# Optimization experiments

Measured on AMD Instinct MI355X. Metric: run time of the kernel, lower is better.

Reference implementation:

```python
import jax, jax.numpy as jnp
import numpy as np

B, T_ENC, T_DEC = 1024, 96, 16
P_Q, CFG, H = 235, 32, 256
D_IN = P_Q + 5 + 10 + 3 + 3  # 256, matches input_size in __init__


def _lstm_step(x, h, c, Wih, Whh, bih, bhh):
    # torch.nn.LSTMCell: gate order i, f, g, o
    g = x @ Wih.T + bih + h @ Whh.T + bhh
    i, f, gg, o = jnp.split(g, 4, axis=-1)
    c2 = jax.nn.sigmoid(f) * c + jax.nn.sigmoid(i) * jnp.tanh(gg)
    h2 = jax.nn.sigmoid(o) * jnp.tanh(c2)
    return h2, c2


def setup_inputs():
    key = jax.random.key(0)
    ks = jax.random.split(key, 30)
    s = 0.05

    def n(i, shape):
        return jax.random.normal(ks[i], shape, jnp.float32) * s

    return {
        "input_p_q": jax.random.normal(ks[0], (B, T_ENC, P_Q), jnp.float32),
        "input_config": jax.random.normal(ks[1], (B, T_ENC, CFG), jnp.float32),
        "input_time": jax.random.randint(ks[2], (B, T_ENC, 3), 0, 5, jnp.int32),
        "W_cfg": n(3, (10, CFG)), "b_cfg": n(4, (10,)),
        "E_hour": n(5, (24, 5)), "E_wd": n(6, (8, 3)), "E_season": n(7, (5, 3)),
        "Wih_e": n(8, (4 * H, D_IN)), "Whh_e": n(9, (4 * H, H)),
        "bih_e": n(10, (4 * H,)), "bhh_e": n(11, (4 * H,)),
        "Wih_d": n(12, (4, H + 1)), "Whh_d": n(13, (4, 1)),
        "bih_d": n(14, (4,)), "bhh_d": n(15, (4,)),
        "Wi_s": n(16, (H, D_IN)), "bi_s": n(17, (H,)),
        "We_s": n(18, (H, 2 * H)),
        "Vd_s": n(19, (1, H)), "bVd_s": n(20, (1,)),
        "Wd_t": n(21, (H, H)), "bd_t": n(22, (H,)),
        "Wd2_t": n(23, (H, 2)),
        "Vd_t": n(24, (1, H)), "bVd_t": n(25, (1,)),
    }


def _forward(input_p_q, input_config, input_time, W_cfg, b_cfg, E_hour, E_wd, E_season,
             Wih_e, Whh_e, bih_e, bhh_e, Wih_d, Whh_d, bih_d, bhh_d,
             Wi_s, bi_s, We_s, Vd_s, bVd_s, Wd_t, bd_t, Wd2_t, Vd_t, bVd_t):
    b = input_p_q.shape[0]
    cfg = input_config @ W_cfg.T + b_cfg  # [B,T,10]
    inputs = jnp.concatenate([
        input_p_q, cfg,
        E_hour[input_time[:, :, 0]],
        E_wd[input_time[:, :, 1]],
        E_season[input_time[:, :, 2]],
    ], axis=2)  # [B,T,D_IN]

    # spatial_attention_Wi(inputs) hoisted out of the per-step loop (identical math)
    wi = inputs @ Wi_s.T + bi_s  # [B,T,H]

    def enc_step(carry, xt):
        hi, ci = carry
        x_t, wi_t = xt
        # Vd(tanh(We([h,c]) + Wi(x)))  -> [B,1] scalar gate (no softmax in original)
        a = jnp.tanh(jnp.concatenate([hi, ci], axis=1) @ We_s.T + wi_t) @ Vd_s.T + bVd_s
        h2, c2 = _lstm_step(x_t * a, hi, ci, Wih_e, Whh_e, bih_e, bhh_e)
        return (h2, c2), h2

    h0 = jnp.zeros((b, H), inputs.dtype)
    (_, _), mid = jax.lax.scan(enc_step, (h0, h0),
                               (inputs.transpose(1, 0, 2), wi.transpose(1, 0, 2)))
    mid = mid.transpose(1, 0, 2)  # [B,T,H]

    # temporal_attention_Wd(mid) does not depend on decode step -> hoisted
    wd_mid = mid @ Wd_t.T + bd_t  # [B,T,H]
    prev0 = mid[:, -1, 2:3]       # [B,1], as in original (element 2 of last hidden)

    def dec_step(carry, _):
        hi, ci, prev = carry
        q = jnp.concatenate([hi, ci], axis=1) @ Wd2_t.T       # [B,H]
        a = jnp.tanh(q[:, None, :] + wd_mid) @ Vd_t.T + bVd_t  # [B,T,1], raw scores
        ctx = jnp.einsum('bth,bt->bh', mid, a[..., 0])          # weighted sum over T
        h2, c2 = _lstm_step(jnp.concatenate([ctx, prev], axis=1), hi, ci,
                            Wih_d, Whh_d, bih_d, bhh_d)
        return (h2, c2, h2), h2

    z = jnp.zeros((b, 1), inputs.dtype)
    _, dec = jax.lax.scan(dec_step, (z, z, prev0), None, length=T_DEC)
    return dec.transpose(1, 0, 2)  # [B,16,1]


def reference(input_p_q, input_config, input_time, W_cfg, b_cfg, E_hour, E_wd, E_season,
              Wih_e, Whh_e, bih_e, bhh_e, Wih_d, Whh_d, bih_d, bhh_d,
              Wi_s, bi_s, We_s, Vd_s, bVd_s, Wd_t, bd_t, Wd2_t, Vd_t, bVd_t):
    return _forward(input_p_q, input_config, input_time, W_cfg, b_cfg, E_hour, E_wd,
                    E_season, Wih_e, Whh_e, bih_e, bhh_e, Wih_d, Whh_d, bih_d, bhh_d,
                    Wi_s, bi_s, We_s, Vd_s, bVd_s, Wd_t, bd_t, Wd2_t, Vd_t, bVd_t)
```

## Files before the change

kernel.cpp:

```cpp
#include <hip/hip_runtime.h>
#include <hip/hip_bf16.h>


typedef unsigned short ushort_t;
using short4v = __attribute__((ext_vector_type(4))) short;
using short8  = __attribute__((ext_vector_type(8))) short;
using floatx4 = __attribute__((ext_vector_type(4))) float;

#define DEVFN static __device__ __forceinline__

DEVFN float bs2f(ushort_t u) {
    union { float f; unsigned v; } c; c.v = ((unsigned)u) << 16; return c.f;
}
DEVFN ushort_t f2bs(float f) {
    __hip_bfloat16 h = __float2bfloat16(f);
    return *reinterpret_cast<ushort_t*>(&h);
}
DEVFN float gload(const void* p, long i, int bf) {
    if (bf) return bs2f(((const ushort_t*)p)[i]);
    return ((const float*)p)[i];
}
DEVFN float sigm(float x) { return 1.f / (1.f + __expf(-x)); }
DEVFN float ftanh(float x) {
    float t = __expf(-2.f * fabsf(x));
    float r = (1.f - t) / (1.f + t);
    return copysignf(r, x);
}
DEVFN short8 ld8(const ushort_t* p) { return *reinterpret_cast<const short8*>(p); }

DEVFN void bar_lgkm() {
    asm volatile("s_waitcnt lgkmcnt(0)" ::: "memory");
    __builtin_amdgcn_s_barrier();
}

DEVFN void gload_lds16(const ushort_t* g, ushort_t* l) {
    typedef const __attribute__((address_space(1))) unsigned int gu32;
    typedef __attribute__((address_space(3))) unsigned int lu32;
    __builtin_amdgcn_global_load_lds((gu32*)g, (lu32*)l, 16, 0, 0);
}

DEVFN const ushort_t* chunk_ptr(const ushort_t* wesW, const ushort_t* whhW, int j) {
    return (j < 16) ? (wesW + (j << 9)) : (whhW + ((j - 16) << 9));
}

struct SrcPtrs { const void* p[26]; };
struct WsPtrs {
    ushort_t *wcfg, *bcfg, *eh, *ew, *es, *wis, *bis, *wes, *vds, *bvds,
             *whh, *wih, *bih, *bhh, *wdt, *bdt, *wd2t, *vdt, *bvdt,
             *wihd, *whhd, *bihd, *bhhd;
};

__global__ void k_detect(const void* probe, int* flag) {
    if (threadIdx.x == 0 && blockIdx.x == 0) {
        const ushort_t* u = (const ushort_t*)probe;
        int ok = 1;
        for (int i = 0; i < 16; ++i) {
            ushort_t v = u[2 * i];
            int e = (v >> 7) & 0xFF;
            if (!(v == 0 || (e >= 96 && e <= 126))) ok = 0;
        }
        *flag = ok;
    }
}

__global__ __launch_bounds__(256) void k_cvt(SrcPtrs sp, WsPtrs wp, const int* flagp) {
    int bf = *flagp;
    const void* src = nullptr; ushort_t* dst = nullptr; long n = 0;
    switch (blockIdx.x) {
        case 0:  src = sp.p[3];  dst = wp.wcfg; n = 320;    break;
        case 1:  src = sp.p[4];  dst = wp.bcfg; n = 10;     break;
        case 2:  src = sp.p[5];  dst = wp.eh;   n = 120;    break;
        case 3:  src = sp.p[6];  dst = wp.ew;   n = 24;     break;
        case 4:  src = sp.p[7];  dst = wp.es;   n = 15;     break;
        case 5:  src = sp.p[16]; dst = wp.wis;  n = 65536;  break;
        case 6:  src = sp.p[17]; dst = wp.bis;  n = 256;    break;
        case 8:  src = sp.p[19]; dst = wp.vds;  n = 256;    break;
        case 9:  src = sp.p[20]; dst = wp.bvds; n = 1;      break;
        case 12: src = sp.p[10]; dst = wp.bih;  n = 1024;   break;
        case 13: src = sp.p[11]; dst = wp.bhh;  n = 1024;   break;
        case 14: src = sp.p[21]; dst = wp.wdt;  n = 65536;  break;
        case 15: src = sp.p[22]; dst = wp.bdt;  n = 256;    break;
        case 16: src = sp.p[23]; dst = wp.wd2t; n = 512;    break;
        case 17: src = sp.p[24]; dst = wp.vdt;  n = 256;    break;
        case 18: src = sp.p[25]; dst = wp.bvdt; n = 1;      break;
        case 19: src = sp.p[12]; dst = wp.wihd; n = 1028;   break;
        case 20: src = sp.p[13]; dst = wp.whhd; n = 4;      break;
        case 21: src = sp.p[14]; dst = wp.bihd; n = 4;      break;
        case 22: src = sp.p[15]; dst = wp.bhhd; n = 4;      break;
        default: return;
    }
    for (long i = threadIdx.x; i < n; i += 256) {
        float v = bf ? bs2f(((const ushort_t*)src)[i]) : ((const float*)src)[i];
        dst[i] = f2bs(v);
    }
}

__global__ __launch_bounds__(256) void k_permA(
    const void* whh_src, const void* wih_src,
    ushort_t* whhp, ushort_t* wihb, const int* flagp)
{
    int bf = *flagp;
    long base = (long)blockIdx.x * 2048;
    if (blockIdx.y == 1) {
#pragma unroll
        for (int ii = 0; ii < 8; ++ii) {
            long p = base + threadIdx.x + ii * 256;
            wihb[p] = f2bs(gload(wih_src, p, bf));
        }
        return;
    }
#pragma unroll
    for (int ii = 0; ii < 8; ++ii) {
        long p = base + threadIdx.x + ii * 256;
        int c = (int)(p >> 9), l = (int)((p >> 3) & 63), e = (int)(p & 7);
        int w = c >> 5, kk = (c >> 2) & 7, g = c & 3;
        int q = l >> 4, ln = l & 15;
        long si = (long)(g * 256 + w * 16 + ln) * 256 + kk * 32 + q * 8 + e;
        whhp[p] = f2bs(gload(whh_src, si, bf));
    }
}

__global__ __launch_bounds__(256) void k_permB(
    const void* wes_src, ushort_t* wesp, const int* flagp)
{
    int bf = *flagp;
    long base = (long)blockIdx.x * 2048;
#pragma unroll
    for (int ii = 0; ii < 8; ++ii) {
        long p = base + threadIdx.x + ii * 256;
        int c = (int)(p >> 9), l = (int)((p >> 3) & 63), e = (int)(p & 7);
        int w = c >> 4, kk = c & 15;
        int q = l >> 4, ln = l & 15;
        long si = (long)(w * 16 + ln) * 512 + kk * 32 + q * 8 + e;
        wesp[p] = f2bs(gload(wes_src, si, bf));
    }
}

__global__ __launch_bounds__(256) void k_build(
    const void* __restrict__ pq, const void* __restrict__ cfg_in,
    const int* __restrict__ timei, WsPtrs wp, const int* __restrict__ flagp,
    ushort_t* __restrict__ inputs)
{
    int bf = *flagp;
    int ch = threadIdx.x;
    for (int rr = 0; rr < 4; ++rr) {
        long row = (long)blockIdx.x * 4 + rr;
        float v;
        if (ch < 235) {
            v = gload(pq, row * 235 + ch, bf);
        } else if (ch < 245) {
            int j = ch - 235;
            float acc = bs2f(wp.bcfg[j]);
            for (int k = 0; k < 32; ++k)
                acc += gload(cfg_in, row * 32 + k, bf) * bs2f(wp.wcfg[j * 32 + k]);
            v = acc;
        } else if (ch < 250) {
            v = bs2f(wp.eh[timei[row * 3 + 0] * 5 + (ch - 245)]);
        } else if (ch < 253) {
            v = bs2f(wp.ew[timei[row * 3 + 1] * 3 + (ch - 250)]);
        } else {
            v = bs2f(wp.es[timei[row * 3 + 2] * 3 + (ch - 253)]);
        }
        inputs[row * 256 + ch] = f2bs(v);
    }
}

__global__ __launch_bounds__(256) void k_gemm(
    const ushort_t* __restrict__ A, const ushort_t* __restrict__ W,
    const ushort_t* __restrict__ bias, ushort_t* __restrict__ out,
    int ostride, int gatherB)
{
    const int K = 256;
    __shared__ alignas(16) ushort_t At[128][40];
    __shared__ alignas(16) ushort_t Bt[128][40];

    int tid  = threadIdx.x;
    int lane = tid & 63, wave = tid >> 6;
    int wm = wave >> 1, wn = wave & 1;
    int q = lane >> 4, ln = lane & 15;
    long mbase = (long)blockIdx.x * 128;

    floatx4 acc[4][4];
#pragma unroll
    for (int i = 0; i < 4; ++i)
#pragma unroll
        for (int j = 0; j < 4; ++j) acc[i][j] = (floatx4){0.f, 0.f, 0.f, 0.f};

    for (int k0 = 0; k0 < K; k0 += 32) {
        __syncthreads();
#pragma unroll
        for (int it = 0; it < 2; ++it) {
            int c = tid + it * 256;
            int r = c >> 2, kc = (c & 3) * 8;
            int wrow = gatherB ? (((r & 3) << 8) + ((int)blockIdx.y << 5) + (r >> 2))
                               : ((int)blockIdx.y * 128 + r);
            *reinterpret_cast<short8*>(&At[r][kc]) = ld8(&A[(mbase + r) * K + k0 + kc]);
            *reinterpret_cast<short8*>(&Bt[r][kc]) = ld8(&W[(long)wrow * K + k0 + kc]);
        }
        __syncthreads();
        short8 af[4];
#pragma unroll
        for (int mt = 0; mt < 4; ++mt)
            af[mt] = *reinterpret_cast<const short8*>(&At[wm * 64 + mt * 16 + ln][q * 8]);
#pragma unroll
        for (int nt = 0; nt < 4; ++nt) {
            short8 bf = *reinterpret_cast<const short8*>(&Bt[wn * 64 + nt * 16 + ln][q * 8]);
#pragma unroll
            for (int mt = 0; mt < 4; ++mt)
                acc[mt][nt] = __builtin_amdgcn_mfma_f32_16x16x32_bf16(af[mt], bf, acc[mt][nt], 0, 0, 0);
        }
    }

#pragma unroll
    for (int mt = 0; mt < 4; ++mt)
#pragma unroll
        for (int nt = 0; nt < 4; ++nt)
#pragma unroll
            for (int reg = 0; reg < 4; ++reg) {
                long row = mbase + wm * 64 + mt * 16 + q * 4 + reg;
                int  col = (int)blockIdx.y * 128 + wn * 64 + nt * 16 + ln;
                float bv = bias ? bs2f(bias[col]) : 0.f;
                out[row * (long)ostride + col] = f2bs(acc[mt][nt][reg] + bv);
            }
}

#define MFMA16(a, b, c) __builtin_amdgcn_mfma_f32_16x16x32_bf16((a), (b), (c), 0, 0, 0)

__global__ __launch_bounds__(1024) void k_encoder(
    const ushort_t* __restrict__ wi, const ushort_t* __restrict__ ax,
    WsPtrs wp, ushort_t* __restrict__ mid)
{
    __shared__ ushort_t wring[16][4][512];
    __shared__ alignas(16) ushort_t hcb[2][16][520];
    __shared__ alignas(16) float aPartT[16][20];

    int tid  = threadIdx.x;
    int lane = tid & 63, w = tid >> 6;
    int q = lane >> 4, ln = lane & 15;
    int u = w * 16 + ln;
    long row0 = (long)blockIdx.x * 16;

    for (int i = tid; i < 2 * 16 * 520; i += 1024) ((ushort_t*)hcb)[i] = 0;

    float bc0 = bs2f(wp.bih[u])       + bs2f(wp.bhh[u]);
    float bc1 = bs2f(wp.bih[256 + u]) + bs2f(wp.bhh[256 + u]);
    float bc2 = bs2f(wp.bih[512 + u]) + bs2f(wp.bhh[512 + u]);
    float bc3 = bs2f(wp.bih[768 + u]) + bs2f(wp.bhh[768 + u]);
    float vds = bs2f(wp.vds[u]);
    float bVd = bs2f(wp.bvds[0]);

    const ushort_t* wesW = wp.wes + ((long)w << 13) + lane * 8;
    const ushort_t* whhW = wp.whh + ((long)w << 14) + lane * 8;

    const ushort_t* wiB[4]; const ushort_t* axB[4];
#pragma unroll
    for (int reg = 0; reg < 4; ++reg) {
        long rw = (row0 + q * 4 + reg) * 96;
        wiB[reg] = wi + rw * 256 + u;
        axB[reg] = ax + rw * 1024 + u * 4;
    }
    int mr = tid >> 6, mc = (tid & 63) * 4;
    ushort_t* midB = mid + (row0 + mr) * 96 * 256 + mc;

    float creg[4] = {0.f, 0.f, 0.f, 0.f};
    __syncthreads();

#pragma unroll
    for (int j = 0; j < 4; ++j)
        gload_lds16(wesW + (j << 9), &wring[w][j][0]);

    for (int t = 0; t < 96; ++t) {
        ushort_t (*R)[520]  = hcb[t & 1];
        ushort_t (*Wb)[520] = hcb[(t & 1) ^ 1];

        {
            long toff = (long)(t > 0 ? t - 1 : 95) * 256;
            uint2 hv = *reinterpret_cast<const uint2*>(&R[mr][mc]);
            *reinterpret_cast<uint2*>(midB + toff) = hv;
        }
        short4v axv[4]; float wiv[4];
#pragma unroll
        for (int reg = 0; reg < 4; ++reg) {
            axv[reg] = *reinterpret_cast<const short4v*>(axB[reg] + (long)t * 1024);
            wiv[reg] = bs2f(wiB[reg][(long)t * 256]);
        }

        floatx4 acc1 = (floatx4){0.f, 0.f, 0.f, 0.f};
#pragma unroll
        for (int kk = 0; kk < 16; ++kk) {
            if (kk < 4) asm volatile("s_waitcnt vmcnt(12)" ::: "memory");
            else        asm volatile("s_waitcnt vmcnt(3)"  ::: "memory");
            short8 bw = ld8(&wring[w][kk & 3][lane * 8]);
            short8 af = ld8(&R[ln][kk * 32 + q * 8]);
            acc1 = MFMA16(af, bw, acc1);
            gload_lds16(chunk_ptr(wesW, whhW, kk + 4), &wring[w][kk & 3][0]);
        }

        float p4[4];
#pragma unroll
        for (int reg = 0; reg < 4; ++reg)
            p4[reg] = ftanh(acc1[reg] + wiv[reg]) * vds;
#pragma unroll
        for (int m = 1; m < 16; m <<= 1) {
#pragma unroll
            for (int reg = 0; reg < 4; ++reg) p4[reg] += __shfl_xor(p4[reg], m, 64);
        }
        if (ln == 0) {
            floatx4 pv = {p4[0], p4[1], p4[2], p4[3]};
            *reinterpret_cast<floatx4*>(&aPartT[w][q * 4]) = pv;
        }
        bar_lgkm();

        floatx4 aH[4];
#pragma unroll
        for (int g = 0; g < 4; ++g) aH[g] = (floatx4){0.f, 0.f, 0.f, 0.f};
#pragma unroll
        for (int kk = 0; kk < 8; ++kk) {
            short8 af = ld8(&R[ln][kk * 32 + q * 8]);
#pragma unroll
            for (int g = 0; g < 4; ++g) {
                const int j  = 16 + kk * 4 + g;
                const int jn = (j + 4 < 48) ? (j + 4) : (j + 4 - 48);
                asm volatile("s_waitcnt vmcnt(3)" ::: "memory");
                short8 bw = ld8(&wring[w][j & 3][lane * 8]);
                aH[g] = MFMA16(af, bw, aH[g]);
                gload_lds16(chunk_ptr(wesW, whhW, jn), &wring[w][j & 3][0]);
            }
        }

        floatx4 av = {bVd, bVd, bVd, bVd};
#pragma unroll
        for (int ww = 0; ww < 16; ++ww)
            av += *reinterpret_cast<const floatx4*>(&aPartT[ww][q * 4]);

#pragma unroll
        for (int reg = 0; reg < 4; ++reg) {
            float a  = av[reg];
            float gi = aH[0][reg] + a * bs2f((ushort_t)axv[reg][0]) + bc0;
            float gf = aH[1][reg] + a * bs2f((ushort_t)axv[reg][1]) + bc1;
            float gg = aH[2][reg] + a * bs2f((ushort_t)axv[reg][2]) + bc2;
            float go = aH[3][reg] + a * bs2f((ushort_t)axv[reg][3]) + bc3;
            float c2 = sigm(gf) * creg[reg] + sigm(gi) * ftanh(gg);
            float h2 = sigm(go) * ftanh(c2);
            creg[reg] = c2;
            int r = q * 4 + reg;
            Wb[r][u] = f2bs(h2);
            Wb[r][256 + u] = f2bs(c2);
        }
        bar_lgkm();
    }

    asm volatile("s_waitcnt vmcnt(0)" ::: "memory");

    {
        uint2 hv = *reinterpret_cast<const uint2*>(&hcb[0][mr][mc]);
        *reinterpret_cast<uint2*>(midB + 95L * 256) = hv;
    }
}

__global__ __launch_bounds__(256) void k_decoder(
    const ushort_t* __restrict__ mid, const ushort_t* __restrict__ wd,
    WsPtrs wp, const int* __restrict__ flagp, void* __restrict__ out)
{
    __shared__ ushort_t wdl[96][264];
    __shared__ float qL[256], aLs[96], ctxL[256], VdtL[256], gL[4];
    __shared__ float st[3];

    int tid = threadIdx.x;
    long b = blockIdx.x;
    int bf = *flagp;

    for (int c = tid; c < 96 * 256; c += 256) {
        int tp = c >> 8, chn = c & 255;
        wdl[tp][chn] = wd[(b * 96 + tp) * 256 + chn];
    }
    qL[tid] = 0.f; ctxL[tid] = 0.f;
    if (tid < 96) aLs[tid] = 0.f;
    if (tid < 4)  gL[tid] = 0.f;
    VdtL[tid] = bs2f(wp.vdt[tid]);
    if (tid == 0) {
        st[0] = 0.f; st[1] = 0.f;
        st[2] = bs2f(mid[(b * 96 + 95) * 256 + 2]);
    }
    float bVdt = bs2f(wp.bvdt[0]);
    float w2a = bs2f(wp.wd2t[tid * 2]), w2b = bs2f(wp.wd2t[tid * 2 + 1]);
    __syncthreads();

    for (int s = 0; s < 16; ++s) {
        float hi = st[0], ci = st[1], prev = st[2];
        qL[tid] = hi * w2a + ci * w2b;
        __syncthreads();
        {
            int v = tid >> 6, l = tid & 63;
            for (int tp = v; tp < 96; tp += 4) {
                float sacc = 0.f;
#pragma unroll
                for (int e = 0; e < 4; ++e) {
                    int u = l * 4 + e;
                    sacc += ftanh(qL[u] + bs2f(wdl[tp][u])) * VdtL[u];
                }
#pragma unroll
                for (int m = 1; m < 64; m <<= 1) sacc += __shfl_xor(sacc, m, 64);
                if (l == 0) aLs[tp] = sacc + bVdt;
            }
        }
        __syncthreads();
        {
            float acc = 0.f;
            for (int tp = 0; tp < 96; ++tp)
                acc += aLs[tp] * bs2f(mid[(b * 96 + tp) * 256 + tid]);
            ctxL[tid] = acc;
        }
        __syncthreads();
        {
            int g = tid >> 6, k = tid & 63;
            float part = 0.f;
#pragma unroll
            for (int e = 0; e < 4; ++e) {
                int u = k + e * 64;
                part += bs2f(wp.wihd[g * 257 + u]) * ctxL[u];
            }
#pragma unroll
            for (int m = 1; m < 64; m <<= 1) part += __shfl_xor(part, m, 64);
            if (k == 0)
                gL[g] = part + bs2f(wp.bihd[g]) + bs2f(wp.bhhd[g])
                      + bs2f(wp.whhd[g]) * hi + bs2f(wp.wihd[g * 257 + 256]) * prev;
        }
        __syncthreads();
        if (tid == 0) {
            float c2 = sigm(gL[1]) * ci + sigm(gL[0]) * ftanh(gL[2]);
            float h2 = sigm(gL[3]) * ftanh(c2);
            st[0] = h2; st[1] = c2; st[2] = h2;
            long oi = b * 16 + s;
            if (bf) ((ushort_t*)out)[oi] = f2bs(h2);
            else    ((float*)out)[oi] = h2;
        }
        __syncthreads();
    }
}

extern "C" void kernel_launch(void* const* d_in, const int* in_sizes, int n_in,
                              void* d_out, int out_size, void* d_ws, size_t ws_size,
                              hipStream_t stream)
{
    const long MT = 1024L * 96;

    int* flagp = (int*)d_ws;
    ushort_t* base = (ushort_t*)((char*)d_ws + 256);

    SrcPtrs sp;
    for (int i = 0; i < 26; ++i) sp.p[i] = d_in[i];

    static const long sizes[23] = {
        320, 10, 120, 24, 15, 65536, 256, 131072, 256, 1,
        262144, 262144, 1024, 1024, 65536, 256, 512, 256, 1,
        1028, 4, 4, 4
    };
    ushort_t* ptrs[23];
    long off = 0;
    for (int i = 0; i < 23; ++i) {
        ptrs[i] = base + off;
        off += (sizes[i] + 7) & ~7L;
    }

    WsPtrs wp;
    wp.wcfg = ptrs[0];  wp.bcfg = ptrs[1];  wp.eh   = ptrs[2];  wp.ew   = ptrs[3];
    wp.es   = ptrs[4];  wp.wis  = ptrs[5];  wp.bis  = ptrs[6];  wp.wes  = ptrs[7];
    wp.vds  = ptrs[8];  wp.bvds = ptrs[9];  wp.whh  = ptrs[10]; wp.wih  = ptrs[11];
    wp.bih  = ptrs[12]; wp.bhh  = ptrs[13]; wp.wdt  = ptrs[14]; wp.bdt  = ptrs[15];
    wp.wd2t = ptrs[16]; wp.vdt  = ptrs[17]; wp.bvdt = ptrs[18]; wp.wihd = ptrs[19];
    wp.whhd = ptrs[20]; wp.bihd = ptrs[21]; wp.bhhd = ptrs[22];

    ushort_t* inputs = base + off;
    ushort_t* wib    = inputs + MT * 256;
    ushort_t* midb   = wib + MT * 256;
    ushort_t* axb    = midb + MT * 256;
    ushort_t* wdb    = wib;

    k_detect<<<1, 64, 0, stream>>>(d_in[3], flagp);
    k_cvt<<<23, 256, 0, stream>>>(sp, wp, flagp);
    k_permA<<<dim3(128, 2), 256, 0, stream>>>(d_in[9], d_in[8], wp.whh, wp.wih, flagp);
    k_permB<<<64, 256, 0, stream>>>(d_in[18], wp.wes, flagp);
    k_build<<<24576, 256, 0, stream>>>(d_in[0], d_in[1], (const int*)d_in[2],
                                       wp, flagp, inputs);
    k_gemm<<<dim3(768, 2), 256, 0, stream>>>(inputs, wp.wis, wp.bis, wib, 256, 0);
    k_gemm<<<dim3(768, 8), 256, 0, stream>>>(inputs, wp.wih, nullptr, axb, 1024, 1);
    k_encoder<<<64, 1024, 0, stream>>>(wib, axb, wp, midb);
    k_gemm<<<dim3(768, 2), 256, 0, stream>>>(midb, wp.wdt, wp.bdt, wdb, 256, 0);
    k_decoder<<<1024, 256, 0, stream>>>(midb, wdb, wp, flagp, d_out);
}
```

Before: 2.550 ms.

## Halve encoder block to 8 waves, each owning two hidden slices with deeper ring

The recurrent encoder kernel now runs 512 threads per block instead of 1024. Each wave computes two 16-unit hidden slices, which doubles its MFMA accumulators and its gate math. Each wave's weight-streaming ring buffer grows from 4 to 12 chunks, with a uniform vmcnt(11) wait, so more global-to-LDS loads are in flight. The goal is to reuse each A-fragment LDS read across two MFMAs, cut the number of waves joining each per-step barrier, and hide weight-load latency better. The cost is higher register pressure and the same total weight traffic spread over fewer waves.

```diff
diff --git a/kernel.cpp b/kernel.cpp
--- a/kernel.cpp
+++ b/kernel.cpp
@@ -39,9 +39,7 @@
     __builtin_amdgcn_global_load_lds((gu32*)g, (lu32*)l, 16, 0, 0);
 }
 
-DEVFN const ushort_t* chunk_ptr(const ushort_t* wesW, const ushort_t* whhW, int j) {
-    return (j < 16) ? (wesW + (j << 9)) : (whhW + ((j - 16) << 9));
-}
+#define VW11() asm volatile("s_waitcnt vmcnt(11)" ::: "memory")
 
 struct SrcPtrs { const void* p[26]; };
 struct WsPtrs {
@@ -226,48 +224,64 @@
 
 #define MFMA16(a, b, c) __builtin_amdgcn_mfma_f32_16x16x32_bf16((a), (b), (c), 0, 0, 0)
 
-__global__ __launch_bounds__(1024) void k_encoder(
+DEVFN const ushort_t* sptr2(const ushort_t* const* wesW, const ushort_t* const* whhW,
+                            int j) {
+    int s = j & 1, c = j >> 1;
+    return (c < 16) ? (wesW[s] + (c << 9)) : (whhW[s] + ((c - 16) << 9));
+}
+
+__global__ __launch_bounds__(512) void k_encoder(
     const ushort_t* __restrict__ wi, const ushort_t* __restrict__ ax,
     WsPtrs wp, ushort_t* __restrict__ mid)
 {
-    __shared__ ushort_t wring[16][4][512];
+    __shared__ ushort_t wring[8][12][512];
     __shared__ alignas(16) ushort_t hcb[2][16][520];
     __shared__ alignas(16) float aPartT[16][20];
 
     int tid  = threadIdx.x;
     int lane = tid & 63, w = tid >> 6;
     int q = lane >> 4, ln = lane & 15;
-    int u = w * 16 + ln;
     long row0 = (long)blockIdx.x * 16;
 
-    for (int i = tid; i < 2 * 16 * 520; i += 1024) ((ushort_t*)hcb)[i] = 0;
-
-    float bc0 = bs2f(wp.bih[u])       + bs2f(wp.bhh[u]);
-    float bc1 = bs2f(wp.bih[256 + u]) + bs2f(wp.bhh[256 + u]);
-    float bc2 = bs2f(wp.bih[512 + u]) + bs2f(wp.bhh[512 + u]);
-    float bc3 = bs2f(wp.bih[768 + u]) + bs2f(wp.bhh[768 + u]);
-    float vds = bs2f(wp.vds[u]);
+    for (int i = tid; i < 2 * 16 * 520; i += 512) ((ushort_t*)hcb)[i] = 0;
+
+    int u0 = w * 32 + ln;
+    float bc[2][4], vds[2];
+#pragma unroll
+    for (int s = 0; s < 2; ++s) {
+        int us = u0 + s * 16;
+        bc[s][0] = bs2f(wp.bih[us])       + bs2f(wp.bhh[us]);
+        bc[s][1] = bs2f(wp.bih[256 + us]) + bs2f(wp.bhh[256 + us]);
+        bc[s][2] = bs2f(wp.bih[512 + us]) + bs2f(wp.bhh[512 + us]);
+        bc[s][3] = bs2f(wp.bih[768 + us]) + bs2f(wp.bhh[768 + us]);
+        vds[s]   = bs2f(wp.vds[us]);
+    }
     float bVd = bs2f(wp.bvds[0]);
 
-    const ushort_t* wesW = wp.wes + ((long)w << 13) + lane * 8;
-    const ushort_t* whhW = wp.whh + ((long)w << 14) + lane * 8;
+    const ushort_t* wesW[2]; const ushort_t* whhW[2];
+#pragma unroll
+    for (int s = 0; s < 2; ++s) {
+        int wprime = 2 * w + s;
+        wesW[s] = wp.wes + ((long)wprime << 13) + lane * 8;
+        whhW[s] = wp.whh + ((long)wprime << 14) + lane * 8;
+    }
 
     const ushort_t* wiB[4]; const ushort_t* axB[4];
 #pragma unroll
     for (int reg = 0; reg < 4; ++reg) {
         long rw = (row0 + q * 4 + reg) * 96;
-        wiB[reg] = wi + rw * 256 + u;
-        axB[reg] = ax + rw * 1024 + u * 4;
-    }
-    int mr = tid >> 6, mc = (tid & 63) * 4;
+        wiB[reg] = wi + rw * 256 + u0;
+        axB[reg] = ax + rw * 1024 + u0 * 4;
+    }
+    int mr = tid >> 5, mc = (tid & 31) * 8;
     ushort_t* midB = mid + (row0 + mr) * 96 * 256 + mc;
 
-    float creg[4] = {0.f, 0.f, 0.f, 0.f};
+    float creg[2][4] = {{0.f, 0.f, 0.f, 0.f}, {0.f, 0.f, 0.f, 0.f}};
     __syncthreads();
 
 #pragma unroll
-    for (int j = 0; j < 4; ++j)
-        gload_lds16(wesW + (j << 9), &wring[w][j][0]);
+    for (int j = 0; j < 12; ++j)
+        gload_lds16(sptr2(wesW, whhW, j), &wring[w][j][0]);
 
     for (int t = 0; t < 96; ++t) {
         ushort_t (*R)[520]  = hcb[t & 1];
@@ -275,56 +289,77 @@
 
         {
             long toff = (long)(t > 0 ? t - 1 : 95) * 256;
-            uint2 hv = *reinterpret_cast<const uint2*>(&R[mr][mc]);
-            *reinterpret_cast<uint2*>(midB + toff) = hv;
-        }
-        short4v axv[4]; float wiv[4];
+            uint4 hv = *reinterpret_cast<const uint4*>(&R[mr][mc]);
+            *reinterpret_cast<uint4*>(midB + toff) = hv;
+        }
+        short4v axv[2][4]; float wiv[2][4];
 #pragma unroll
         for (int reg = 0; reg < 4; ++reg) {
-            axv[reg] = *reinterpret_cast<const short4v*>(axB[reg] + (long)t * 1024);
-            wiv[reg] = bs2f(wiB[reg][(long)t * 256]);
-        }
-
-        floatx4 acc1 = (floatx4){0.f, 0.f, 0.f, 0.f};
+            const ushort_t* a0 = axB[reg] + (long)t * 1024;
+            axv[0][reg] = *reinterpret_cast<const short4v*>(a0);
+            axv[1][reg] = *reinterpret_cast<const short4v*>(a0 + 64);
+            const ushort_t* w0 = wiB[reg] + (long)t * 256;
+            wiv[0][reg] = bs2f(w0[0]);
+            wiv[1][reg] = bs2f(w0[16]);
+        }
+
+        floatx4 acc1[2];
+        acc1[0] = (floatx4){0.f, 0.f, 0.f, 0.f};
+        acc1[1] = (floatx4){0.f, 0.f, 0.f, 0.f};
 #pragma unroll
         for (int kk = 0; kk < 16; ++kk) {
-            if (kk < 4) asm volatile("s_waitcnt vmcnt(12)" ::: "memory");
-            else        asm volatile("s_waitcnt vmcnt(3)"  ::: "memory");
-            short8 bw = ld8(&wring[w][kk & 3][lane * 8]);
             short8 af = ld8(&R[ln][kk * 32 + q * 8]);
-            acc1 = MFMA16(af, bw, acc1);
-            gload_lds16(chunk_ptr(wesW, whhW, kk + 4), &wring[w][kk & 3][0]);
-        }
-
-        float p4[4];
-#pragma unroll
-        for (int reg = 0; reg < 4; ++reg)
-            p4[reg] = ftanh(acc1[reg] + wiv[reg]) * vds;
+#pragma unroll
+            for (int s = 0; s < 2; ++s) {
+                const int j = kk * 2 + s;
+                VW11();
+                short8 bw = ld8(&wring[w][j % 12][lane * 8]);
+                acc1[s] = MFMA16(af, bw, acc1[s]);
+                gload_lds16(sptr2(wesW, whhW, (j + 12) % 96), &wring[w][j % 12][0]);
+            }
+        }
+
+        float p4[2][4];
+#pragma unroll
+        for (int s = 0; s < 2; ++s)
+#pragma unroll
+            for (int reg = 0; reg < 4; ++reg)
+                p4[s][reg] = ftanh(acc1[s][reg] + wiv[s][reg]) * vds[s];
 #pragma unroll
         for (int m = 1; m < 16; m <<= 1) {
 #pragma unroll
-            for (int reg = 0; reg < 4; ++reg) p4[reg] += __shfl_xor(p4[reg], m, 64);
+            for (int s = 0; s < 2; ++s)
+#pragma unroll
+                for (int reg = 0; reg < 4; ++reg)
+                    p4[s][reg] += __shfl_xor(p4[s][reg], m, 64);
         }
         if (ln == 0) {
-            floatx4 pv = {p4[0], p4[1], p4[2], p4[3]};
-            *reinterpret_cast<floatx4*>(&aPartT[w][q * 4]) = pv;
+#pragma unroll
+            for (int s = 0; s < 2; ++s) {
+                floatx4 pv = {p4[s][0], p4[s][1], p4[s][2], p4[s][3]};
+                *reinterpret_cast<floatx4*>(&aPartT[2 * w + s][q * 4]) = pv;
+            }
         }
         bar_lgkm();
 
-        floatx4 aH[4];
-#pragma unroll
-        for (int g = 0; g < 4; ++g) aH[g] = (floatx4){0.f, 0.f, 0.f, 0.f};
+        floatx4 aH[2][4];
+#pragma unroll
+        for (int s = 0; s < 2; ++s)
+#pragma unroll
+            for (int g = 0; g < 4; ++g) aH[s][g] = (floatx4){0.f, 0.f, 0.f, 0.f};
 #pragma unroll
         for (int kk = 0; kk < 8; ++kk) {
             short8 af = ld8(&R[ln][kk * 32 + q * 8]);
 #pragma unroll
             for (int g = 0; g < 4; ++g) {
-                const int j  = 16 + kk * 4 + g;
-                const int jn = (j + 4 < 48) ? (j + 4) : (j + 4 - 48);
-                asm volatile("s_waitcnt vmcnt(3)" ::: "memory");
-                short8 bw = ld8(&wring[w][j & 3][lane * 8]);
-                aH[g] = MFMA16(af, bw, aH[g]);
-                gload_lds16(chunk_ptr(wesW, whhW, jn), &wring[w][j & 3][0]);
+#pragma unroll
+                for (int s = 0; s < 2; ++s) {
+                    const int j = 32 + (kk * 4 + g) * 2 + s;
+                    VW11();
+                    short8 bw = ld8(&wring[w][j % 12][lane * 8]);
+                    aH[s][g] = MFMA16(af, bw, aH[s][g]);
+                    gload_lds16(sptr2(wesW, whhW, (j + 12) % 96), &wring[w][j % 12][0]);
+                }
             }
         }
 
@@ -334,27 +369,30 @@
             av += *reinterpret_cast<const floatx4*>(&aPartT[ww][q * 4]);
 
 #pragma unroll
-        for (int reg = 0; reg < 4; ++reg) {
-            float a  = av[reg];
-            float gi = aH[0][reg] + a * bs2f((ushort_t)axv[reg][0]) + bc0;
-            float gf = aH[1][reg] + a * bs2f((ushort_t)axv[reg][1]) + bc1;
-            float gg = aH[2][reg] + a * bs2f((ushort_t)axv[reg][2]) + bc2;
-            float go = aH[3][reg] + a * bs2f((ushort_t)axv[reg][3]) + bc3;
-            float c2 = sigm(gf) * creg[reg] + sigm(gi) * ftanh(gg);
-            float h2 = sigm(go) * ftanh(c2);
-            creg[reg] = c2;
-            int r = q * 4 + reg;
-            Wb[r][u] = f2bs(h2);
-            Wb[r][256 + u] = f2bs(c2);
+        for (int s = 0; s < 2; ++s) {
+            int us = u0 + s * 16;
+#pragma unroll
+            for (int reg = 0; reg < 4; ++reg) {
+                float a  = av[reg];
+                float gi = aH[s][0][reg] + a * bs2f((ushort_t)axv[s][reg][0]) + bc[s][0];
+                float gf = aH[s][1][reg] + a * bs2f((ushort_t)axv[s][reg][1]) + bc[s][1];
+                float gg = aH[s][2][reg] + a * bs2f((ushort_t)axv[s][reg][2]) + bc[s][2];
+                float go = aH[s][3][reg] + a * bs2f((ushort_t)axv[s][reg][3]) + bc[s][3];
+                float c2 = sigm(gf) * creg[s][reg] + sigm(gi) * ftanh(gg);
+                float h2 = sigm(go) * ftanh(c2);
+                creg[s][reg] = c2;
+                int r = q * 4 + reg;
+                Wb[r][us] = f2bs(h2);
+                Wb[r][256 + us] = f2bs(c2);
+            }
         }
         bar_lgkm();
     }
 
     asm volatile("s_waitcnt vmcnt(0)" ::: "memory");
-
     {
-        uint2 hv = *reinterpret_cast<const uint2*>(&hcb[0][mr][mc]);
-        *reinterpret_cast<uint2*>(midB + 95L * 256) = hv;
+        uint4 hv = *reinterpret_cast<const uint4*>(&hcb[0][mr][mc]);
+        *reinterpret_cast<uint4*>(midB + 95L * 256) = hv;
     }
 }
 
@@ -485,7 +523,7 @@
                                        wp, flagp, inputs);
     k_gemm<<<dim3(768, 2), 256, 0, stream>>>(inputs, wp.wis, wp.bis, wib, 256, 0);
     k_gemm<<<dim3(768, 8), 256, 0, stream>>>(inputs, wp.wih, nullptr, axb, 1024, 1);
-    k_encoder<<<64, 1024, 0, stream>>>(wib, axb, wp, midb);
+    k_encoder<<<64, 512, 0, stream>>>(wib, axb, wp, midb);
     k_gemm<<<dim3(768, 2), 256, 0, stream>>>(midb, wp.wdt, wp.bdt, wdb, 256, 0);
     k_decoder<<<1024, 256, 0, stream>>>(midb, wdb, wp, flagp, d_out);
 }
```

Result: faster. 2.483 ms (-2.6%).
